# Kernel tuning notes

Measured on AMD Instinct MI355X. Metric: run time of the kernel, lower is better.

## Reference

```python
import math
import jax, jax.numpy as jnp
import numpy as np

B, L, D = 2, 2048, 1024
NH = 16
HS = D // NH
BLOCK_SIZE = 2048


def setup_inputs() -> dict:
    key = jax.random.key(0)
    ks = jax.random.split(key, 4)
    x = jax.random.normal(ks[0], (B, L, D), dtype=jnp.float32)
    Wqkv = jax.random.normal(ks[1], (D, 3 * D), dtype=jnp.float32) * 0.02
    bqkv = jnp.zeros((3 * D,), dtype=jnp.float32)
    Wproj = jax.random.normal(ks[2], (D, D), dtype=jnp.float32) * 0.02
    bproj = jnp.zeros((D,), dtype=jnp.float32)
    Er = jax.random.normal(ks[3], (BLOCK_SIZE, HS), dtype=jnp.float32)
    return {"x": x, "Wqkv": Wqkv, "bqkv": bqkv, "Wproj": Wproj, "bproj": bproj, "Er": Er}


def _skew(QEr):
    # QEr: [B, nh, L, L]  (Music Transformer skew trick)
    b, nh, nr, nc = QEr.shape
    padded = jnp.pad(QEr, ((0, 0), (0, 0), (0, 0), (1, 0)))  # [B, nh, nr, nc+1]
    reshaped = padded.reshape(b, nh, nc + 1, nr)
    return reshaped[:, :, 1:, :]  # [B, nh, nr, nc]


def reference(x, Wqkv, bqkv, Wproj, bproj, Er):
    b, l, d = x.shape
    qkv = x @ Wqkv + bqkv  # [B, L, 3D]
    q, k, v = jnp.split(qkv, 3, axis=2)
    q = q.reshape(b, l, NH, HS).transpose(0, 2, 1, 3)  # [B, nh, L, hs]
    k = k.reshape(b, l, NH, HS).transpose(0, 2, 1, 3)
    v = v.reshape(b, l, NH, HS).transpose(0, 2, 1, 3)

    start = BLOCK_SIZE - l
    Er_t = Er[start:, :].T  # [hs, L]
    QEr = jnp.einsum('bhld,dm->bhlm', q, Er_t)  # [B, nh, L, L]
    Srel = _skew(QEr)

    QK_t = jnp.einsum('bhld,bhmd->bhlm', q, k)
    scale = 1.0 / math.sqrt(HS)
    att = (QK_t + Srel) * scale
    causal = jnp.tril(jnp.ones((l, l), dtype=bool))
    att = jnp.where(causal[None, None, :, :], att, jnp.float32(-jnp.inf))
    att = jax.nn.softmax(att, axis=-1)
    y = jnp.einsum('bhlm,bhmd->bhld', att, v)
    y = y.transpose(0, 2, 1, 3).reshape(b, l, d)
    return y @ Wproj + bproj
```

## Files before the change

kernel.cpp:

```cpp
#include <hip/hip_runtime.h>
#include <stdint.h>

#define BB 2
#define LL 2048
#define DD 1024
#define NHH 16
#define HSS 64

typedef __bf16 bf16x8 __attribute__((ext_vector_type(8)));
typedef float f32x4 __attribute__((ext_vector_type(4)));

__device__ __forceinline__ bf16x8 load8(const float* p) {
  float4 f0 = *(const float4*)p;
  float4 f1 = *(const float4*)(p + 4);
  bf16x8 v;
  v[0] = (__bf16)f0.x; v[1] = (__bf16)f0.y; v[2] = (__bf16)f0.z; v[3] = (__bf16)f0.w;
  v[4] = (__bf16)f1.x; v[5] = (__bf16)f1.y; v[6] = (__bf16)f1.z; v[7] = (__bf16)f1.w;
  return v;
}
__device__ __forceinline__ bf16x8 load8(const __bf16* p) {
  return *(const bf16x8*)p;
}

__device__ __forceinline__ void async_ld16(__bf16* lds_uniform_base,
                                           const __bf16* gptr_per_lane) {
  __builtin_amdgcn_global_load_lds(
      (const __attribute__((address_space(1))) void*)gptr_per_lane,
      (__attribute__((address_space(3))) void*)lds_uniform_base, 16, 0, 0);
}

__global__ void prep_k(const float* __restrict__ Wqkv, const float* __restrict__ x,
                       const float* __restrict__ Er, __bf16* __restrict__ WqkvT,
                       __bf16* __restrict__ xb, __bf16* __restrict__ Erb) {
  int tx = threadIdx.x, ty = threadIdx.y;
  int tid = ty * 32 + tx;
  if (blockIdx.z == 1) {
    if (blockIdx.x >= 2048) return;
    size_t off = ((size_t)blockIdx.x * 256 + tid) * 8;
    *(bf16x8*)&xb[off] = load8(&x[off]);
    return;
  }
  if (blockIdx.z == 2) {
    if (blockIdx.x >= 64) return;
    size_t off = ((size_t)blockIdx.x * 256 + tid) * 8;
    *(bf16x8*)&Erb[off] = load8(&Er[off]);
    return;
  }
  __shared__ __bf16 tile[32][33];
  int c0 = (blockIdx.x % 96) * 32, r0 = (blockIdx.x / 96) * 32;
#pragma unroll
  for (int i = ty; i < 32; i += 8)
    tile[i][tx] = (__bf16)Wqkv[(size_t)(r0 + i) * 3072 + c0 + tx];
  __syncthreads();
#pragma unroll
  for (int i = ty; i < 32; i += 8)
    WqkvT[(size_t)(c0 + i) * 1024 + r0 + tx] = tile[tx][i];
}

__global__ __launch_bounds__(256) void gemm_qkv_k(
    const __bf16* __restrict__ A, const __bf16* __restrict__ Bt,
    const float* __restrict__ bias, __bf16* __restrict__ Qo,
    __bf16* __restrict__ Ko, __bf16* __restrict__ Vto) {
  const int K = 1024;
  __shared__ __align__(16) __bf16 As[128 * 32];
  __shared__ __align__(16) __bf16 Bs[128 * 32];
  int t = threadIdx.x;
  int wave = t >> 6, lane = t & 63, qd = lane >> 4, lr = lane & 15;
  int m0 = blockIdx.y * 128, n0 = blockIdx.x * 128;
  int wm = (wave >> 1) * 64, wn = (wave & 1) * 64;
  f32x4 acc[4][4] = {};
  int srow = lane >> 2, sch = (lane & 3) * 8;
  const __bf16* Ab[2];
  const __bf16* Bb[2];
#pragma unroll
  for (int c = 0; c < 2; c++) {
    Ab[c] = A + (size_t)(m0 + (wave * 2 + c) * 16 + srow) * K + sch;
    Bb[c] = Bt + (size_t)(n0 + (wave * 2 + c) * 16 + srow) * K + sch;
  }
  for (int k0 = 0; k0 < K; k0 += 32) {
    __syncthreads();
#pragma unroll
    for (int c = 0; c < 2; c++) {
      async_ld16(&As[(wave * 2 + c) * 512], Ab[c] + k0);
      async_ld16(&Bs[(wave * 2 + c) * 512], Bb[c] + k0);
    }
    __syncthreads();
    bf16x8 af[4], bfr[4];
#pragma unroll
    for (int mt = 0; mt < 4; mt++)
      af[mt] = *(const bf16x8*)&As[(wm + mt * 16 + lr) * 32 + qd * 8];
#pragma unroll
    for (int nt = 0; nt < 4; nt++)
      bfr[nt] = *(const bf16x8*)&Bs[(wn + nt * 16 + lr) * 32 + qd * 8];
#pragma unroll
    for (int mt = 0; mt < 4; mt++)
#pragma unroll
      for (int nt = 0; nt < 4; nt++)
        acc[mt][nt] = __builtin_amdgcn_mfma_f32_16x16x32_bf16(af[mt], bfr[nt],
                                                              acc[mt][nt], 0, 0, 0);
  }
  float bvv[4];
#pragma unroll
  for (int nt = 0; nt < 4; nt++) bvv[nt] = bias[n0 + wn + nt * 16 + lr];
#pragma unroll
  for (int mt = 0; mt < 4; mt++)
#pragma unroll
    for (int nt = 0; nt < 4; nt++)
#pragma unroll
      for (int r = 0; r < 4; r++) {
        int row = m0 + wm + mt * 16 + qd * 4 + r;
        int col = n0 + wn + nt * 16 + lr;
        __bf16 bb = (__bf16)(acc[mt][nt][r] + bvv[nt]);
        int b = row >> 11, l = row & 2047;
        int h = (col >> 6) & 15, d = col & 63;
        if (col < DD) {
          Qo[(((size_t)(b * NHH + h)) * LL + l) * HSS + d] = bb;
        } else if (col < 2 * DD) {
          Ko[(((size_t)(b * NHH + h)) * LL + l) * HSS + d] = bb;
        } else {
          Vto[(((size_t)(b * NHH + h)) * HSS + d) * LL + l] = bb;
        }
      }
}

__global__ __launch_bounds__(256) void gemm_proj_k(
    const __bf16* __restrict__ A, const float* __restrict__ Bg,
    const float* __restrict__ bias, float* __restrict__ out) {
  const int K = 1024, N = 1024;
  __shared__ __align__(16) __bf16 As[128 * 32];
  __shared__ __align__(16) __bf16 Bs[64 * 40];
  int t = threadIdx.x;
  int wave = t >> 6, lane = t & 63, qd = lane >> 4, lr = lane & 15;
  int m0 = blockIdx.y * 128, n0 = blockIdx.x * 64;
  int wm = (wave >> 1) * 64, wn = (wave & 1) * 32;
  f32x4 acc[4][2] = {};
  int srow = lane >> 2, sch = (lane & 3) * 8;
  const __bf16* Ab[2];
#pragma unroll
  for (int c = 0; c < 2; c++)
    Ab[c] = A + (size_t)(m0 + (wave * 2 + c) * 16 + srow) * K + sch;
  int kk = t >> 3, nn = (t & 7) * 8;
  const float* Bp = Bg + (size_t)kk * N + n0 + nn;

  for (int k0 = 0; k0 < K; k0 += 32) {
    __syncthreads();
#pragma unroll
    for (int c = 0; c < 2; c++)
      async_ld16(&As[(wave * 2 + c) * 512], Ab[c] + k0);
    bf16x8 bv = load8(Bp + (size_t)k0 * N);
#pragma unroll
    for (int j = 0; j < 8; j++) Bs[(nn + j) * 40 + kk] = bv[j];
    __syncthreads();
    bf16x8 af[4], bfr[2];
#pragma unroll
    for (int mt = 0; mt < 4; mt++)
      af[mt] = *(const bf16x8*)&As[(wm + mt * 16 + lr) * 32 + qd * 8];
#pragma unroll
    for (int nt = 0; nt < 2; nt++)
      bfr[nt] = *(const bf16x8*)&Bs[(wn + nt * 16 + lr) * 40 + qd * 8];
#pragma unroll
    for (int mt = 0; mt < 4; mt++)
#pragma unroll
      for (int nt = 0; nt < 2; nt++)
        acc[mt][nt] = __builtin_amdgcn_mfma_f32_16x16x32_bf16(af[mt], bfr[nt],
                                                              acc[mt][nt], 0, 0, 0);
  }
  float bvv[2];
#pragma unroll
  for (int nt = 0; nt < 2; nt++) bvv[nt] = bias[n0 + wn + nt * 16 + lr];
#pragma unroll
  for (int mt = 0; mt < 4; mt++)
#pragma unroll
    for (int nt = 0; nt < 2; nt++)
#pragma unroll
      for (int r = 0; r < 4; r++) {
        int row = m0 + wm + mt * 16 + qd * 4 + r;
        int col = n0 + wn + nt * 16 + lr;
        out[(size_t)row * N + col] = acc[mt][nt][r] + bvv[nt];
      }
}

__global__ __launch_bounds__(256, 3) void flash_k(
    const __bf16* __restrict__ Qg, const __bf16* __restrict__ Kg,
    const __bf16* __restrict__ Vtg, const __bf16* __restrict__ Erb,
    __bf16* __restrict__ Yg) {
  __shared__ __align__(16) __bf16 Kld[64 * 72];
  __shared__ __align__(16) __bf16 Vld[80 * 72];
  __shared__ __align__(16) __bf16 Pball[4][16 * 72];

  int bh = blockIdx.x;
  int i0 = (31 - (int)blockIdx.y) * 64;
  const __bf16* Qh = Qg + (size_t)bh * LL * HSS;
  const __bf16* Kh = Kg + (size_t)bh * LL * HSS;
  const __bf16* Vth = Vtg + (size_t)bh * HSS * LL;
  int b = bh >> 4, h = bh & 15;
  int t = threadIdx.x, wave = t >> 6, lane = t & 63, qd = lane >> 4, lr = lane & 15;
  __bf16* Pb = &Pball[wave][0];
  int cbase = 48 - wave * 16;

  for (int idx = t; idx < 16 * 72; idx += 256) {
    int rr = idx / 72;
    Vld[(64 + rr) * 72 + (idx - rr * 72)] = (rr == 0) ? (__bf16)1.f : (__bf16)0.f;
  }

  int jj = t >> 2, hf = t & 3;

  bf16x8 aq[2];
  {
    const __bf16* qrow = Qh + (size_t)(i0 + wave * 16 + lr) * HSS + qd * 8;
    aq[0] = *(const bf16x8*)qrow;
    aq[1] = *(const bf16x8*)(qrow + 32);
  }
  f32x4 oacc[5] = {};

  bf16x8 kr0, kr1, vr0, vr1;
  auto prefetch = [&](int j0) {
    kr0 = *(const bf16x8*)&Kh[(size_t)(j0 + jj) * HSS + hf * 16];
    kr1 = *(const bf16x8*)&Kh[(size_t)(j0 + jj) * HSS + hf * 16 + 8];
    vr0 = *(const bf16x8*)&Vth[(size_t)jj * LL + j0 + hf * 16];
    vr1 = *(const bf16x8*)&Vth[(size_t)jj * LL + j0 + hf * 16 + 8];
  };
  prefetch(0);

  for (int j0 = 0; j0 <= i0; j0 += 64) {
    __syncthreads();
    *(bf16x8*)&Kld[jj * 72 + hf * 16] = kr0;
    *(bf16x8*)&Kld[jj * 72 + hf * 16 + 8] = kr1;
    *(bf16x8*)&Vld[jj * 72 + hf * 16] = vr0;
    *(bf16x8*)&Vld[jj * 72 + hf * 16 + 8] = vr1;
    __syncthreads();
    if (j0 + 64 <= i0) prefetch(j0 + 64);

    bf16x8 ef[5][2];
    int ebase = LL - 64 - i0 + j0 + cbase;
#pragma unroll
    for (int ct = 0; ct < 5; ct++) {
      int e = ebase + ct * 16 + lr;
      e = (e < LL) ? e : (LL - 1);
#pragma unroll
      for (int kc = 0; kc < 2; kc++)
        ef[ct][kc] = *(const bf16x8*)&Erb[(size_t)e * HSS + kc * 32 + qd * 8];
    }

    f32x4 sacc[4] = {};
#pragma unroll
    for (int ct = 0; ct < 4; ct++)
#pragma unroll
      for (int kc = 0; kc < 2; kc++) {
        bf16x8 bk = *(const bf16x8*)&Kld[(ct * 16 + lr) * 72 + kc * 32 + qd * 8];
        sacc[ct] = __builtin_amdgcn_mfma_f32_16x16x32_bf16(aq[kc], bk, sacc[ct], 0, 0, 0);
      }
    f32x4 racc[5] = {};
#pragma unroll
    for (int ct = 0; ct < 5; ct++)
#pragma unroll
      for (int kc = 0; kc < 2; kc++)
        racc[ct] = __builtin_amdgcn_mfma_f32_16x16x32_bf16(aq[kc], ef[ct][kc],
                                                           racc[ct], 0, 0, 0);

#pragma unroll
    for (int r = 0; r < 4; r++) {
      int tr = qd * 4 + r;
      int base = 15 - tr + lr;
      int src = qd * 16 + (base & 15);
      int hi = base >> 4;
      float sh[5];
#pragma unroll
      for (int ct = 0; ct < 5; ct++) sh[ct] = __shfl(racc[ct][r], src, 64);
      int gi = i0 + wave * 16 + tr;
#pragma unroll
      for (int ct2 = 0; ct2 < 4; ct2++) {
        float rel = hi ? sh[ct2 + 1] : sh[ct2];
        float s = (sacc[ct2][r] + rel) * 0.125f;
        int gj = j0 + ct2 * 16 + lr;
        float p = (gj <= gi) ? __expf(s) : 0.f;
        Pb[tr * 72 + ct2 * 16 + lr] = (__bf16)p;
      }
    }

    bf16x8 ap0 = *(const bf16x8*)&Pb[lr * 72 + qd * 8];
    bf16x8 ap1 = *(const bf16x8*)&Pb[lr * 72 + 32 + qd * 8];
#pragma unroll
    for (int dt = 0; dt < 5; dt++) {
      bf16x8 bv0 = *(const bf16x8*)&Vld[(dt * 16 + lr) * 72 + qd * 8];
      bf16x8 bv1 = *(const bf16x8*)&Vld[(dt * 16 + lr) * 72 + 32 + qd * 8];
      oacc[dt] = __builtin_amdgcn_mfma_f32_16x16x32_bf16(ap0, bv0, oacc[dt], 0, 0, 0);
      oacc[dt] = __builtin_amdgcn_mfma_f32_16x16x32_bf16(ap1, bv1, oacc[dt], 0, 0, 0);
    }
  }

#pragma unroll
  for (int r = 0; r < 4; r++) {
    float lv = __shfl(oacc[4][r], qd * 16, 64);
    float inv = 1.f / lv;
    int l = i0 + wave * 16 + qd * 4 + r;
#pragma unroll
    for (int dt = 0; dt < 4; dt++) {
      int d = dt * 16 + lr;
      Yg[((size_t)(b * LL) + l) * DD + h * HSS + d] = (__bf16)(oacc[dt][r] * inv);
    }
  }
}

extern "C" void kernel_launch(void* const* d_in, const int* in_sizes, int n_in,
                              void* d_out, int out_size, void* d_ws, size_t ws_size,
                              hipStream_t stream) {
  const float* x = (const float*)d_in[0];
  const float* Wqkv = (const float*)d_in[1];
  const float* bqkv = (const float*)d_in[2];
  const float* Wproj = (const float*)d_in[3];
  const float* bproj = (const float*)d_in[4];
  const float* Er = (const float*)d_in[5];
  float* out = (float*)d_out;

  if (ws_size < 4u * 8388608u) return;

  uint8_t* w = (uint8_t*)d_ws;
  __bf16* Q = (__bf16*)w;  w += (size_t)BB * NHH * LL * HSS * 2;
  __bf16* Kt = (__bf16*)w; w += (size_t)BB * NHH * LL * HSS * 2;
  __bf16* Vt = (__bf16*)w; w += (size_t)BB * NHH * LL * HSS * 2;
  __bf16* Y = (__bf16*)w;  w += (size_t)BB * LL * DD * 2;

  __bf16* WqkvT = (__bf16*)d_out;
  __bf16* xb = (__bf16*)((uint8_t*)d_out + (size_t)3072 * 1024 * 2);
  __bf16* Erb = (__bf16*)((uint8_t*)d_out + (size_t)3072 * 1024 * 2 + (size_t)4096 * 1024 * 2);

  prep_k<<<dim3(3072, 1, 3), dim3(32, 8), 0, stream>>>(Wqkv, x, Er, WqkvT, xb, Erb);
  gemm_qkv_k<<<dim3(3072 / 128, 4096 / 128), 256, 0, stream>>>(
      xb, WqkvT, bqkv, Q, Kt, Vt);
  flash_k<<<dim3(BB * NHH, 32), 256, 0, stream>>>(Q, Kt, Vt, Erb, Y);
  gemm_proj_k<<<dim3(1024 / 64, 4096 / 128), 256, 0, stream>>>(Y, Wproj, bproj, out);
}
```

Measured before the change: 263.8 us.

## Pre-transpose Wproj to bf16 and shrink flash LDS with register ones-vector

Adds a transpose-convert kernel that writes Wproj as bf16 [N,K] into the now-dead Q buffer, so the projection GEMM can stage B with async 16-byte loads instead of per-element transposed LDS stores. In flash attention, the ones-rows used to compute the softmax row sum are now held in a register vector rather than an extra 16 LDS rows of V. The smaller LDS footprint lets the launch-bounds occupancy hint rise from 3 to 4 blocks. The cost is one extra small kernel launch and higher register pressure under the tighter occupancy target.

Result: no change. 265.7 us (+0.7%).

```diff
diff --git a/kernel.cpp b/kernel.cpp
--- a/kernel.cpp
+++ b/kernel.cpp
@@ -55,6 +55,20 @@
 #pragma unroll
   for (int i = ty; i < 32; i += 8)
     WqkvT[(size_t)(c0 + i) * 1024 + r0 + tx] = tile[tx][i];
+}
+
+__global__ void tconv_k(const float* __restrict__ src, __bf16* __restrict__ dst,
+                        int R, int C) {
+  __shared__ __bf16 tile[32][33];
+  int c0 = blockIdx.x * 32, r0 = blockIdx.y * 32;
+  int tx = threadIdx.x, ty = threadIdx.y;
+#pragma unroll
+  for (int i = ty; i < 32; i += 8)
+    tile[i][tx] = (__bf16)src[(size_t)(r0 + i) * C + c0 + tx];
+  __syncthreads();
+#pragma unroll
+  for (int i = ty; i < 32; i += 8)
+    dst[(size_t)(c0 + i) * R + r0 + tx] = tile[tx][i];
 }
 
 __global__ __launch_bounds__(256) void gemm_qkv_k(
@@ -124,11 +138,11 @@
 }
 
 __global__ __launch_bounds__(256) void gemm_proj_k(
-    const __bf16* __restrict__ A, const float* __restrict__ Bg,
+    const __bf16* __restrict__ A, const __bf16* __restrict__ Bt,
     const float* __restrict__ bias, float* __restrict__ out) {
   const int K = 1024, N = 1024;
   __shared__ __align__(16) __bf16 As[128 * 32];
-  __shared__ __align__(16) __bf16 Bs[64 * 40];
+  __shared__ __align__(16) __bf16 Bs[64 * 32];
   int t = threadIdx.x;
   int wave = t >> 6, lane = t & 63, qd = lane >> 4, lr = lane & 15;
   int m0 = blockIdx.y * 128, n0 = blockIdx.x * 64;
@@ -136,20 +150,18 @@
   f32x4 acc[4][2] = {};
   int srow = lane >> 2, sch = (lane & 3) * 8;
   const __bf16* Ab[2];
+  const __bf16* Bb;
 #pragma unroll
   for (int c = 0; c < 2; c++)
     Ab[c] = A + (size_t)(m0 + (wave * 2 + c) * 16 + srow) * K + sch;
-  int kk = t >> 3, nn = (t & 7) * 8;
-  const float* Bp = Bg + (size_t)kk * N + n0 + nn;
+  Bb = Bt + (size_t)(n0 + wave * 16 + srow) * K + sch;
 
   for (int k0 = 0; k0 < K; k0 += 32) {
     __syncthreads();
 #pragma unroll
     for (int c = 0; c < 2; c++)
       async_ld16(&As[(wave * 2 + c) * 512], Ab[c] + k0);
-    bf16x8 bv = load8(Bp + (size_t)k0 * N);
-#pragma unroll
-    for (int j = 0; j < 8; j++) Bs[(nn + j) * 40 + kk] = bv[j];
+    async_ld16(&Bs[wave * 512], Bb + k0);
     __syncthreads();
     bf16x8 af[4], bfr[2];
 #pragma unroll
@@ -157,7 +169,7 @@
       af[mt] = *(const bf16x8*)&As[(wm + mt * 16 + lr) * 32 + qd * 8];
 #pragma unroll
     for (int nt = 0; nt < 2; nt++)
-      bfr[nt] = *(const bf16x8*)&Bs[(wn + nt * 16 + lr) * 40 + qd * 8];
+      bfr[nt] = *(const bf16x8*)&Bs[(wn + nt * 16 + lr) * 32 + qd * 8];
 #pragma unroll
     for (int mt = 0; mt < 4; mt++)
 #pragma unroll
@@ -180,12 +192,12 @@
       }
 }
 
-__global__ __launch_bounds__(256, 3) void flash_k(
+__global__ __launch_bounds__(256, 4) void flash_k(
     const __bf16* __restrict__ Qg, const __bf16* __restrict__ Kg,
     const __bf16* __restrict__ Vtg, const __bf16* __restrict__ Erb,
     __bf16* __restrict__ Yg) {
   __shared__ __align__(16) __bf16 Kld[64 * 72];
-  __shared__ __align__(16) __bf16 Vld[80 * 72];
+  __shared__ __align__(16) __bf16 Vld[64 * 72];
   __shared__ __align__(16) __bf16 Pball[4][16 * 72];
 
   int bh = blockIdx.x;
@@ -198,10 +210,9 @@
   __bf16* Pb = &Pball[wave][0];
   int cbase = 48 - wave * 16;
 
-  for (int idx = t; idx < 16 * 72; idx += 256) {
-    int rr = idx / 72;
-    Vld[(64 + rr) * 72 + (idx - rr * 72)] = (rr == 0) ? (__bf16)1.f : (__bf16)0.f;
-  }
+  bf16x8 bones;
+#pragma unroll
+  for (int q = 0; q < 8; q++) bones[q] = (lr == 0) ? (__bf16)1.f : (__bf16)0.f;
 
   int jj = t >> 2, hf = t & 3;
 
@@ -281,12 +292,14 @@
     bf16x8 ap0 = *(const bf16x8*)&Pb[lr * 72 + qd * 8];
     bf16x8 ap1 = *(const bf16x8*)&Pb[lr * 72 + 32 + qd * 8];
 #pragma unroll
-    for (int dt = 0; dt < 5; dt++) {
+    for (int dt = 0; dt < 4; dt++) {
       bf16x8 bv0 = *(const bf16x8*)&Vld[(dt * 16 + lr) * 72 + qd * 8];
       bf16x8 bv1 = *(const bf16x8*)&Vld[(dt * 16 + lr) * 72 + 32 + qd * 8];
       oacc[dt] = __builtin_amdgcn_mfma_f32_16x16x32_bf16(ap0, bv0, oacc[dt], 0, 0, 0);
       oacc[dt] = __builtin_amdgcn_mfma_f32_16x16x32_bf16(ap1, bv1, oacc[dt], 0, 0, 0);
     }
+    oacc[4] = __builtin_amdgcn_mfma_f32_16x16x32_bf16(ap0, bones, oacc[4], 0, 0, 0);
+    oacc[4] = __builtin_amdgcn_mfma_f32_16x16x32_bf16(ap1, bones, oacc[4], 0, 0, 0);
   }
 
 #pragma unroll
@@ -324,10 +337,12 @@
   __bf16* WqkvT = (__bf16*)d_out;
   __bf16* xb = (__bf16*)((uint8_t*)d_out + (size_t)3072 * 1024 * 2);
   __bf16* Erb = (__bf16*)((uint8_t*)d_out + (size_t)3072 * 1024 * 2 + (size_t)4096 * 1024 * 2);
+  __bf16* WprojT = Q;
 
   prep_k<<<dim3(3072, 1, 3), dim3(32, 8), 0, stream>>>(Wqkv, x, Er, WqkvT, xb, Erb);
   gemm_qkv_k<<<dim3(3072 / 128, 4096 / 128), 256, 0, stream>>>(
       xb, WqkvT, bqkv, Q, Kt, Vt);
   flash_k<<<dim3(BB * NHH, 32), 256, 0, stream>>>(Q, Kt, Vt, Erb, Y);
-  gemm_proj_k<<<dim3(1024 / 64, 4096 / 128), 256, 0, stream>>>(Y, Wproj, bproj, out);
-}
+  tconv_k<<<dim3(1024 / 32, 1024 / 32), dim3(32, 8), 0, stream>>>(Wproj, WprojT, 1024, 1024);
+  gemm_proj_k<<<dim3(1024 / 64, 4096 / 128), 256, 0, stream>>>(Y, WprojT, bproj, out);
+}
```
